# Performance work log

Hardware: AMD Instinct MI355X
Metric: run time of the kernel (lower is better)

The kernel has to match this reference:

```python
import jax, jax.numpy as jnp
import numpy as np

B, S, D, H, DK, DV = 2, 2048, 1024, 16, 64, 64
NEG_INF = -2.0**32 + 1.0  # matches torch module's self.inf


def setup_inputs() -> dict:
    key = jax.random.key(0)
    ks = jax.random.split(key, 9)
    sc = 0.02
    x = jax.random.normal(ks[0], (B, S, D), jnp.float32)
    Wq = jax.random.normal(ks[1], (D, H * DK), jnp.float32) * sc
    bq = jax.random.normal(ks[2], (H * DK,), jnp.float32) * sc
    Wk = jax.random.normal(ks[3], (D, H * DK), jnp.float32) * sc
    bk = jax.random.normal(ks[4], (H * DK,), jnp.float32) * sc
    Wv = jax.random.normal(ks[5], (D, H * DV), jnp.float32) * sc
    bv = jax.random.normal(ks[6], (H * DV,), jnp.float32) * sc
    Wo = jax.random.normal(ks[7], (H * DV, D), jnp.float32) * sc
    bo = jax.random.normal(ks[8], (D,), jnp.float32) * sc
    return {"x": x, "Wq": Wq, "bq": bq, "Wk": Wk, "bk": bk,
            "Wv": Wv, "bv": bv, "Wo": Wo, "bo": bo}


def reference(x, Wq, bq, Wk, bk, Wv, bv, Wo, bo):
    # stage == 'train' path: causal mask applied.
    b, s, _ = x.shape
    # chunk(heads, dim=-1) + cat(dim=0) in torch == per-head split; equivalent
    # math expressed as [B, S, H, d] with head-batched einsums.
    q = (x @ Wq + bq).reshape(b, s, H, DK)
    k = (x @ Wk + bk).reshape(b, s, H, DK)
    v = (x @ Wv + bv).reshape(b, s, H, DV)
    # NOTE: original module does NOT scale by 1/sqrt(dk) — stay faithful.
    score = jnp.einsum('bqhd,bkhd->bhqk', q, k)  # [B, H, S, S]
    causal = jnp.tril(jnp.ones((s, s), dtype=bool))
    score = jnp.where(causal, score, NEG_INF)
    attn = jax.nn.softmax(score, axis=-1)
    ctx = jnp.einsum('bhqk,bkhd->bqhd', attn, v).reshape(b, s, H * DV)
    return ctx @ Wo + bo
```

## Files before the change

### kernel.cpp

```cpp
#include <hip/hip_runtime.h>
#include <stdint.h>

typedef unsigned short u16;
typedef __bf16 bf16_t;
typedef bf16_t bf16x8 __attribute__((ext_vector_type(8)));
typedef float f32x4 __attribute__((ext_vector_type(4)));

#define SB 2048
#define DMODEL 1024
#define NH 16
#define HD 64

__device__ __forceinline__ u16 f2bf(float f) {
  union { float f; uint32_t u; } v; v.f = f;
  uint32_t u = v.u;
  return (u16)((u + 0x7FFFu + ((u >> 16) & 1u)) >> 16);
}

__device__ __forceinline__ void gload16(const void* g, void* l) {
  __builtin_amdgcn_global_load_lds((const __attribute__((address_space(1))) void*)g,
                                   (__attribute__((address_space(3))) void*)l, 16, 0, 0);
}


__global__ __launch_bounds__(256) void k_cvt_x(const float* __restrict__ x, u16* __restrict__ xb) {
  int i = blockIdx.x * 256 + threadIdx.x;
  float4 v = ((const float4*)x)[i];
  uint2 o;
  o.x = (unsigned)f2bf(v.x) | ((unsigned)f2bf(v.y) << 16);
  o.y = (unsigned)f2bf(v.z) | ((unsigned)f2bf(v.w) << 16);
  ((uint2*)xb)[i] = o;
}

__global__ __launch_bounds__(256) void k_transpose_w(
    const float* __restrict__ W0, const float* __restrict__ W1,
    const float* __restrict__ W2, const float* __restrict__ W3,
    u16* __restrict__ T0, u16* __restrict__ T1,
    u16* __restrict__ T2, u16* __restrict__ T3) {
  __shared__ float tile[32][33];
  int mat = blockIdx.z;
  const float* W = (mat == 0) ? W0 : (mat == 1) ? W1 : (mat == 2) ? W2 : W3;
  u16* T = (mat == 0) ? T0 : (mat == 1) ? T1 : (mat == 2) ? T2 : T3;
  int r0 = blockIdx.y * 32, c0 = blockIdx.x * 32;
  int tx = threadIdx.x & 31, ty = threadIdx.x >> 5;
#pragma unroll
  for (int j = 0; j < 4; ++j)
    tile[ty + j * 8][tx] = W[(size_t)(r0 + ty + j * 8) * DMODEL + c0 + tx];
  __syncthreads();
#pragma unroll
  for (int j = 0; j < 4; ++j)
    T[(size_t)(c0 + ty + j * 8) * DMODEL + r0 + tx] = f2bf(tile[tx][ty + j * 8]);
}


#define STG(MATBASE, LDS, SLOT, HALF, TK)                                          \
  do {                                                                             \
    _Pragma("unroll") for (int q_ = 0; q_ < 2; ++q_) {                             \
      int glin_ = tid + q_ * 512;                                                  \
      int row_ = glin_ >> 3;                                                       \
      int g_ = (glin_ & 7) ^ (row_ & 7);                                           \
      gload16(MATBASE + (size_t)((HALF) * 128 + row_) * DMODEL + (TK) * 64 + g_ * 8, \
              &LDS[SLOT][(HALF) * 8192 + glin_ * 8]);                              \
    }                                                                              \
  } while (0)

#define RDA(SLOT, MH)                                                     \
  do {                                                                    \
    _Pragma("unroll") for (int mm_ = 0; mm_ < 4; ++mm_) {                 \
      _Pragma("unroll") for (int kk_ = 0; kk_ < 2; ++kk_) {               \
        int row_ = wr * 128 + ((MH) * 4 + mm_) * 16 + l15;                \
        int g_ = (kk_ * 4 + grp) ^ (row_ & 7);                            \
        a[mm_][kk_] = *(const bf16x8*)&As[SLOT][row_ * 64 + g_ * 8];      \
      }                                                                   \
    }                                                                     \
  } while (0)

#define RDB(SLOT, NHF)                                                    \
  do {                                                                    \
    _Pragma("unroll") for (int nn_ = 0; nn_ < 2; ++nn_) {                 \
      _Pragma("unroll") for (int kk_ = 0; kk_ < 2; ++kk_) {               \
        int n_ = (NHF) * 2 + nn_;                                         \
        int row_ = wc * 64 + n_ * 16 + l15;                               \
        int g_ = (kk_ * 4 + grp) ^ (row_ & 7);                            \
        b[n_][kk_] = *(const bf16x8*)&Bs[SLOT][row_ * 64 + g_ * 8];       \
      }                                                                   \
    }                                                                     \
  } while (0)

#define MFM(MH, NHF)                                                                    \
  do {                                                                                  \
    _Pragma("unroll") for (int mm_ = 0; mm_ < 4; ++mm_) {                               \
      _Pragma("unroll") for (int nn_ = 0; nn_ < 2; ++nn_) {                             \
        _Pragma("unroll") for (int kk_ = 0; kk_ < 2; ++kk_) {                           \
          acc[(MH) * 4 + mm_][(NHF) * 2 + nn_] = __builtin_amdgcn_mfma_f32_16x16x32_bf16( \
              a[mm_][kk_], b[(NHF) * 2 + nn_][kk_], acc[(MH) * 4 + mm_][(NHF) * 2 + nn_], \
              0, 0, 0);                                                                 \
        }                                                                               \
      }                                                                                 \
    }                                                                                   \
  } while (0)

#define SBAR()                             \
  do {                                     \
    __builtin_amdgcn_sched_barrier(0);     \
    __builtin_amdgcn_s_barrier();          \
    __builtin_amdgcn_sched_barrier(0);     \
  } while (0)

#define LGKM0()                                           \
  do {                                                    \
    asm volatile("s_waitcnt lgkmcnt(0)" ::: "memory");    \
    __builtin_amdgcn_sched_barrier(0);                    \
  } while (0)

#define VMW(N)                                                \
  do {                                                        \
    asm volatile("s_waitcnt vmcnt(" #N ")" ::: "memory");     \
    __builtin_amdgcn_sched_barrier(0);                        \
  } while (0)

#define PHASE(RD0, RD1, ISS, MH, NHF, WAITC) \
  do {                                       \
    RD0;                                     \
    RD1;                                     \
    ISS;                                     \
    SBAR();                                  \
    LGKM0();                                 \
    __builtin_amdgcn_s_setprio(1);           \
    MFM(MH, NHF);                            \
    __builtin_amdgcn_s_setprio(0);           \
    WAITC;                                   \
    SBAR();                                  \
  } while (0)

__global__ __launch_bounds__(512, 2) void k_qkv8(
    const u16* __restrict__ xb, const u16* __restrict__ WqT, const u16* __restrict__ WkT,
    const u16* __restrict__ WvT, const float* __restrict__ bq, const float* __restrict__ bk,
    const float* __restrict__ bv, u16* __restrict__ Qg, u16* __restrict__ Kg,
    u16* __restrict__ VTg) {
  __shared__ u16 As[2][16384];
  __shared__ u16 Bs[2][16384];
  const int tid = threadIdx.x, w = tid >> 6, lane = tid & 63;
  const int l15 = lane & 15, grp = lane >> 4;
  const int wr = w >> 2, wc = w & 3;

  int id = blockIdx.x;
  id = (id & 7) * 24 + (id >> 3);
  const int role_v = (id >= 128);
  int mt, ntb;
  const u16 *Abase, *Bbase;
  if (!role_v) {
    mt = id >> 3;
    ntb = id & 7;
    Abase = xb + (size_t)mt * 256 * DMODEL;
    Bbase = (ntb < 4 ? WqT : WkT) + (size_t)(ntb & 3) * 256 * DMODEL;
  } else {
    int v = id - 128;
    mt = v >> 4;
    ntb = v & 15;
    Abase = WvT + (size_t)mt * 256 * DMODEL;
    Bbase = xb + (size_t)ntb * 256 * DMODEL;
  }

  f32x4 acc[8][4];
#pragma unroll
  for (int m = 0; m < 8; ++m)
#pragma unroll
    for (int n = 0; n < 4; ++n) acc[m][n] = (f32x4){0.f, 0.f, 0.f, 0.f};

  STG(Abase, As, 0, 0, 0);
  STG(Bbase, Bs, 0, 0, 0);
  STG(Abase, As, 0, 1, 0);
  STG(Bbase, Bs, 0, 1, 0);
  STG(Bbase, Bs, 1, 0, 1);
  STG(Abase, As, 1, 0, 1);
  VMW(4);
  SBAR();

  bf16x8 a[4][2], b[4][2];
#pragma unroll 1
  for (int it = 0; it < 8; ++it) {
    const int t0 = it * 2;
    const bool s2 = (t0 + 2) < 16, s3 = (t0 + 3) < 16;
    PHASE(RDA(0, 0), RDB(0, 0), STG(Bbase, Bs, 1, 1, t0 + 1), 0, 0, );
    PHASE(RDB(0, 1), , STG(Abase, As, 1, 1, t0 + 1), 0, 1, );
    PHASE(RDA(0, 1), , if (s2) STG(Bbase, Bs, 0, 0, t0 + 2), 1, 0, );
    PHASE(, , if (s2) STG(Abase, As, 0, 0, t0 + 2), 1, 1, if (s2) VMW(4); else VMW(0));
    PHASE(RDA(1, 0), RDB(1, 0), if (s2) STG(Bbase, Bs, 0, 1, t0 + 2), 0, 0, );
    PHASE(RDB(1, 1), , if (s2) STG(Abase, As, 0, 1, t0 + 2), 0, 1, );
    PHASE(RDA(1, 1), , if (s3) STG(Bbase, Bs, 1, 0, t0 + 3), 1, 0, );
    PHASE(, , if (s3) STG(Abase, As, 1, 0, t0 + 3), 1, 1, if (s3) VMW(4));
  }

#pragma unroll
  for (int m = 0; m < 8; ++m)
#pragma unroll
    for (int n = 0; n < 4; ++n)
#pragma unroll
      for (int r = 0; r < 4; ++r) {
        int mr = wr * 128 + m * 16 + 4 * grp + r;
        int nc = wc * 64 + n * 16 + l15;
        float v = acc[m][n][r];
        if (!role_v) {
          int Ng = ntb * 256 + nc;
          int col = Ng & 1023;
          float vb = v + (Ng < 1024 ? bq[col] : bk[col]);
          int mrow = mt * 256 + mr;
          int b_ = mrow >> 11, s_ = mrow & 2047, h_ = col >> 6, d_ = col & 63;
          u16* out = (Ng < 1024) ? Qg : Kg;
          out[((((size_t)b_ * NH + h_) * SB + s_) << 6) + d_] = f2bf(vb);
        } else {
          int vcf = mt * 256 + mr;
          int seq = ntb * 256 + nc;
          float vb = v + bv[vcf];
          int b2 = seq >> 11, key = seq & 2047, h2 = vcf >> 6, vc = vcf & 63;
          VTg[((((size_t)b2 * NH + h2) << 6) + vc) * SB + key] = f2bf(vb);
        }
      }
}


__device__ __forceinline__ void gemm_loop(const u16* __restrict__ A, const u16* __restrict__ Bt,
                                          u16* As, u16* Bs, f32x4 (&acc)[4][4], int m0) {
  const int t = threadIdx.x, w = t >> 6, lane = t & 63;
  const int l15 = lane & 15, grp = lane >> 4;
  const int wr = w >> 1, wc = w & 1;
#pragma unroll
  for (int i = 0; i < 4; ++i)
#pragma unroll
    for (int j = 0; j < 4; ++j) acc[i][j] = (f32x4){0.f, 0.f, 0.f, 0.f};

  for (int ks = 0; ks < 16; ++ks) {
    const int k0 = ks * 64;
#pragma unroll
    for (int j = 0; j < 4; ++j) {
      int glin = (w * 4 + j) * 64 + lane;
      int row = glin >> 3;
      int g = (glin & 7) ^ (row & 7);
      gload16(A + (size_t)(m0 + row) * DMODEL + k0 + g * 8, (char*)As + (size_t)(w * 4 + j) * 1024);
      gload16(Bt + (size_t)row * DMODEL + k0 + g * 8, (char*)Bs + (size_t)(w * 4 + j) * 1024);
    }
    __syncthreads();
#pragma unroll
    for (int kk = 0; kk < 2; ++kk) {
      bf16x8 af[4], bfr[4];
#pragma unroll
      for (int i = 0; i < 4; ++i) {
        int row = wr * 64 + i * 16 + l15;
        int g = (4 * kk + grp) ^ (row & 7);
        af[i] = *(const bf16x8*)((const char*)As + row * 128 + (g << 4));
      }
#pragma unroll
      for (int j = 0; j < 4; ++j) {
        int row = wc * 64 + j * 16 + l15;
        int g = (4 * kk + grp) ^ (row & 7);
        bfr[j] = *(const bf16x8*)((const char*)Bs + row * 128 + (g << 4));
      }
#pragma unroll
      for (int i = 0; i < 4; ++i)
#pragma unroll
        for (int j = 0; j < 4; ++j)
          acc[i][j] = __builtin_amdgcn_mfma_f32_16x16x32_bf16(af[i], bfr[j], acc[i][j], 0, 0, 0);
    }
    __syncthreads();
  }
}

__global__ __launch_bounds__(256) void k_gemm_o(
    const u16* __restrict__ ctx, const u16* __restrict__ WoT,
    const float* __restrict__ bo, float* __restrict__ out) {
  __shared__ u16 As[128 * 64];
  __shared__ u16 Bs[128 * 64];
  const int nt = blockIdx.x, mt = blockIdx.y;
  const int n0 = nt * 128;

  f32x4 acc[4][4];
  gemm_loop(ctx, WoT + (size_t)n0 * DMODEL, As, Bs, acc, mt * 128);

  const int t = threadIdx.x, w = t >> 6, lane = t & 63;
  const int l15 = lane & 15, grp = lane >> 4;
  const int wr = w >> 1, wc = w & 1;
#pragma unroll
  for (int i = 0; i < 4; ++i)
#pragma unroll
    for (int j = 0; j < 4; ++j)
#pragma unroll
      for (int r = 0; r < 4; ++r) {
        int mrow = mt * 128 + wr * 64 + i * 16 + 4 * grp + r;
        int ncol = n0 + wc * 64 + j * 16 + l15;
        out[(size_t)mrow * DMODEL + ncol] = acc[i][j][r] + bo[ncol];
      }
}


__global__ __launch_bounds__(256) void k_flash(const u16* __restrict__ Qg,
                                               const u16* __restrict__ Kg,
                                               const u16* __restrict__ VTg,
                                               u16* __restrict__ ctx) {
  __shared__ u16 Ks[2][64 * 64];
  __shared__ u16 VTs[2][64 * 64];
  __shared__ u16 Ps[4][16 * 64];
  const int linb = blockIdx.x;
  const int xcd = linb & 7, idx = linb >> 3;
  const int bh = xcd + ((idx & 3) << 3);
  const int pi = idx >> 2;
  const int t = threadIdx.x, w = t >> 6, lane = t & 63;
  const int l15 = lane & 15, grp = lane >> 4;
  const size_t bhS = (size_t)bh * SB;
  const u16* Kb = Kg + (bhS << 6);
  const u16* Vb = VTg + (bhS << 6);
  const int b = bh >> 4, h = bh & 15;

#pragma unroll 1
  for (int ph = 0; ph < 2; ++ph) {
    const int qt = ph ? 31 - pi : pi;
    const int qb = qt * 64;
    bf16x8 qf[2];
#pragma unroll
    for (int c = 0; c < 2; ++c)
      qf[c] = *(const bf16x8*)(Qg + ((bhS + qb + w * 16 + l15) << 6) + 32 * c + 8 * grp);
    f32x4 acc[4];
    float plsum[4];
#pragma unroll
    for (int ct = 0; ct < 4; ++ct) acc[ct] = (f32x4){0.f, 0.f, 0.f, 0.f};
#pragma unroll
    for (int j = 0; j < 4; ++j) plsum[j] = 0.f;

#pragma unroll
    for (int j = 0; j < 2; ++j) {
      int glin = w * 128 + j * 64 + lane;
      int row = glin >> 3;
      int g = (glin & 7) ^ (row & 7);
      gload16(Kb + ((size_t)row << 6) + g * 8, (char*)Ks[0] + w * 2048 + j * 1024);
      gload16(Vb + ((size_t)row << 11) + g * 8, (char*)VTs[0] + w * 2048 + j * 1024);
    }
    __syncthreads();
    int cur = 0;
    for (int kt = 0; kt <= qt; ++kt) {
      if (kt < qt) {
        const int kb2 = (kt + 1) * 64;
#pragma unroll
        for (int j = 0; j < 2; ++j) {
          int glin = w * 128 + j * 64 + lane;
          int row = glin >> 3;
          int g = (glin & 7) ^ (row & 7);
          gload16(Kb + ((size_t)(kb2 + row) << 6) + g * 8,
                  (char*)Ks[cur ^ 1] + w * 2048 + j * 1024);
          gload16(Vb + ((size_t)row << 11) + kb2 + g * 8,
                  (char*)VTs[cur ^ 1] + w * 2048 + j * 1024);
        }
      }
      f32x4 sc[4];
#pragma unroll
      for (int ct = 0; ct < 4; ++ct) {
        sc[ct] = (f32x4){0.f, 0.f, 0.f, 0.f};
#pragma unroll
        for (int c = 0; c < 2; ++c) {
          int row = ct * 16 + l15;
          int g = (4 * c + grp) ^ (row & 7);
          bf16x8 kf = *(const bf16x8*)((const char*)Ks[cur] + row * 128 + (g << 4));
          sc[ct] = __builtin_amdgcn_mfma_f32_16x16x32_bf16(qf[c], kf, sc[ct], 0, 0, 0);
        }
      }
      if (kt == qt) {
#pragma unroll
        for (int ct = 0; ct < 4; ++ct)
#pragma unroll
          for (int j = 0; j < 4; ++j) {
            int key = ct * 16 + l15, r = w * 16 + 4 * grp + j;
            if (key > r) sc[ct][j] = -1e30f;
          }
      }
#pragma unroll
      for (int ct = 0; ct < 4; ++ct)
#pragma unroll
        for (int j = 0; j < 4; ++j) {
          float p = __expf(sc[ct][j] - 32.0f);
          plsum[j] += p;
          int r = 4 * grp + j, cc = ct * 16 + l15;
          *(u16*)((char*)Ps[w] + r * 128 + (((cc >> 3) ^ (r & 7)) << 4) + (cc & 7) * 2) = f2bf(p);
        }
      asm volatile("s_waitcnt lgkmcnt(0)" ::: "memory");
      __builtin_amdgcn_sched_barrier(0);
#pragma unroll
      for (int ct = 0; ct < 4; ++ct) {
#pragma unroll
        for (int c2 = 0; c2 < 2; ++c2) {
          int pg = (4 * c2 + grp) ^ (l15 & 7);
          bf16x8 pf = *(const bf16x8*)((const char*)Ps[w] + l15 * 128 + (pg << 4));
          int vrow = ct * 16 + l15;
          int vg = (4 * c2 + grp) ^ (vrow & 7);
          bf16x8 vf = *(const bf16x8*)((const char*)VTs[cur] + vrow * 128 + (vg << 4));
          acc[ct] = __builtin_amdgcn_mfma_f32_16x16x32_bf16(pf, vf, acc[ct], 0, 0, 0);
        }
      }
      __syncthreads();
      cur ^= 1;
    }
#pragma unroll
    for (int j = 0; j < 4; ++j) {
#pragma unroll
      for (int d = 1; d < 16; d <<= 1) plsum[j] += __shfl_xor(plsum[j], d, 64);
      float inv = 1.f / plsum[j];
      int rg = qb + w * 16 + 4 * grp + j;
#pragma unroll
      for (int ct = 0; ct < 4; ++ct) {
        int col = h * 64 + ct * 16 + l15;
        ctx[((size_t)b * SB + rg) * DMODEL + col] = f2bf(acc[ct][j] * inv);
      }
    }
  }
}


extern "C" void kernel_launch(void* const* d_in, const int* in_sizes, int n_in,
                              void* d_out, int out_size, void* d_ws, size_t ws_size,
                              hipStream_t stream) {
  const float* x  = (const float*)d_in[0];
  const float* Wq = (const float*)d_in[1];
  const float* bq = (const float*)d_in[2];
  const float* Wk = (const float*)d_in[3];
  const float* bk = (const float*)d_in[4];
  const float* Wv = (const float*)d_in[5];
  const float* bv = (const float*)d_in[6];
  const float* Wo = (const float*)d_in[7];
  const float* bo = (const float*)d_in[8];
  float* out = (float*)d_out;

  char* ws = (char*)d_ws;
  u16* xb  = (u16*)(ws);
  u16* WqT = (u16*)(ws + (8ull  << 20));
  u16* WkT = (u16*)(ws + (10ull << 20));
  u16* WvT = (u16*)(ws + (12ull << 20));
  u16* WoT = (u16*)(ws + (14ull << 20));
  u16* Qg  = (u16*)(ws + (16ull << 20));
  u16* Kg  = (u16*)(ws + (24ull << 20));
  u16* VTg = (u16*)(ws + (32ull << 20));
  u16* ctx = (u16*)(ws + (40ull << 20));

  hipLaunchKernelGGL(k_cvt_x, dim3(4096), dim3(256), 0, stream, x, xb);
  hipLaunchKernelGGL(k_transpose_w, dim3(32, 32, 4), dim3(256), 0, stream,
                     Wq, Wk, Wv, Wo, WqT, WkT, WvT, WoT);
  hipLaunchKernelGGL(k_qkv8, dim3(192), dim3(512), 0, stream,
                     xb, WqT, WkT, WvT, bq, bk, bv, Qg, Kg, VTg);
  hipLaunchKernelGGL(k_flash, dim3(512), dim3(256), 0, stream, Qg, Kg, VTg, ctx);
  hipLaunchKernelGGL(k_gemm_o, dim3(8, 32), dim3(256), 0, stream, ctx, WoT, bo, out);
}
```

Measured before the change: 130.6 us.

## Use 128-row query tiles with 8 waves in flash attention kernel

The flash attention kernel now processes 128 query rows per block using 512 threads (8 waves), halving the grid to 256 blocks. Each K/V tile loaded into shared memory is therefore reused by twice as many query rows, and each thread issues one load per tile instead of two. The causal mask check becomes per-wave, since a 64-key tile may partly overlap a 128-row query block. Separately, sched_barrier fences around s_barrier and vmcnt waits in the QKV GEMM macros are dropped, and the output GEMM pointer arithmetic is simplified. The trade-offs are fewer resident blocks, and waves whose rows lie entirely below the last key tile doing wasted masked work on that tile.

After: 132.7 us. Within noise of the previous version (+1.6%).

```diff
diff --git a/kernel.cpp b/kernel.cpp
--- a/kernel.cpp
+++ b/kernel.cpp
@@ -100,12 +100,7 @@
     }                                                                                   \
   } while (0)
 
-#define SBAR()                             \
-  do {                                     \
-    __builtin_amdgcn_sched_barrier(0);     \
-    __builtin_amdgcn_s_barrier();          \
-    __builtin_amdgcn_sched_barrier(0);     \
-  } while (0)
+#define SBAR() __builtin_amdgcn_s_barrier()
 
 #define LGKM0()                                           \
   do {                                                    \
@@ -113,11 +108,7 @@
     __builtin_amdgcn_sched_barrier(0);                    \
   } while (0)
 
-#define VMW(N)                                                \
-  do {                                                        \
-    asm volatile("s_waitcnt vmcnt(" #N ")" ::: "memory");     \
-    __builtin_amdgcn_sched_barrier(0);                        \
-  } while (0)
+#define VMW(N) asm volatile("s_waitcnt vmcnt(" #N ")" ::: "memory")
 
 #define PHASE(RD0, RD1, ISS, MH, NHF, WAITC) \
   do {                                       \
@@ -221,7 +212,7 @@
 
 
 __device__ __forceinline__ void gemm_loop(const u16* __restrict__ A, const u16* __restrict__ Bt,
-                                          u16* As, u16* Bs, f32x4 (&acc)[4][4], int m0) {
+                                          u16* As, u16* Bs, f32x4 (&acc)[4][4]) {
   const int t = threadIdx.x, w = t >> 6, lane = t & 63;
   const int l15 = lane & 15, grp = lane >> 4;
   const int wr = w >> 1, wc = w & 1;
@@ -237,7 +228,7 @@
       int glin = (w * 4 + j) * 64 + lane;
       int row = glin >> 3;
       int g = (glin & 7) ^ (row & 7);
-      gload16(A + (size_t)(m0 + row) * DMODEL + k0 + g * 8, (char*)As + (size_t)(w * 4 + j) * 1024);
+      gload16(A + (size_t)row * DMODEL + k0 + g * 8, (char*)As + (size_t)(w * 4 + j) * 1024);
       gload16(Bt + (size_t)row * DMODEL + k0 + g * 8, (char*)Bs + (size_t)(w * 4 + j) * 1024);
     }
     __syncthreads();
@@ -272,10 +263,9 @@
   __shared__ u16 As[128 * 64];
   __shared__ u16 Bs[128 * 64];
   const int nt = blockIdx.x, mt = blockIdx.y;
-  const int n0 = nt * 128;
 
   f32x4 acc[4][4];
-  gemm_loop(ctx, WoT + (size_t)n0 * DMODEL, As, Bs, acc, mt * 128);
+  gemm_loop(ctx + (size_t)mt * 128 * DMODEL, WoT + (size_t)nt * 128 * DMODEL, As, Bs, acc);
 
   const int t = threadIdx.x, w = t >> 6, lane = t & 63;
   const int l15 = lane & 15, grp = lane >> 4;
@@ -287,19 +277,19 @@
 #pragma unroll
       for (int r = 0; r < 4; ++r) {
         int mrow = mt * 128 + wr * 64 + i * 16 + 4 * grp + r;
-        int ncol = n0 + wc * 64 + j * 16 + l15;
+        int ncol = nt * 128 + wc * 64 + j * 16 + l15;
         out[(size_t)mrow * DMODEL + ncol] = acc[i][j][r] + bo[ncol];
       }
 }
 
 
-__global__ __launch_bounds__(256) void k_flash(const u16* __restrict__ Qg,
+__global__ __launch_bounds__(512) void k_flash(const u16* __restrict__ Qg,
                                                const u16* __restrict__ Kg,
                                                const u16* __restrict__ VTg,
                                                u16* __restrict__ ctx) {
-  __shared__ u16 Ks[2][64 * 64];
-  __shared__ u16 VTs[2][64 * 64];
-  __shared__ u16 Ps[4][16 * 64];
+  __shared__ u16 Ks[2][4096];
+  __shared__ u16 VTs[2][4096];
+  __shared__ u16 Ps[8][1024];
   const int linb = blockIdx.x;
   const int xcd = linb & 7, idx = linb >> 3;
   const int bh = xcd + ((idx & 3) << 3);
@@ -313,8 +303,9 @@
 
 #pragma unroll 1
   for (int ph = 0; ph < 2; ++ph) {
-    const int qt = ph ? 31 - pi : pi;
-    const int qb = qt * 64;
+    const int qt = ph ? 15 - pi : pi;
+    const int qb = qt * 128;
+    const int nkt = 2 * qt + 2;
     bf16x8 qf[2];
 #pragma unroll
     for (int c = 0; c < 2; ++c)
@@ -326,29 +317,20 @@
 #pragma unroll
     for (int j = 0; j < 4; ++j) plsum[j] = 0.f;
 
-#pragma unroll
-    for (int j = 0; j < 2; ++j) {
-      int glin = w * 128 + j * 64 + lane;
-      int row = glin >> 3;
-      int g = (glin & 7) ^ (row & 7);
-      gload16(Kb + ((size_t)row << 6) + g * 8, (char*)Ks[0] + w * 2048 + j * 1024);
-      gload16(Vb + ((size_t)row << 11) + g * 8, (char*)VTs[0] + w * 2048 + j * 1024);
+    {
+      int row = t >> 3, g = (t & 7) ^ (row & 7);
+      gload16(Kb + ((size_t)row << 6) + g * 8, (char*)Ks[0] + t * 16);
+      gload16(Vb + ((size_t)row << 11) + g * 8, (char*)VTs[0] + t * 16);
     }
     __syncthreads();
     int cur = 0;
-    for (int kt = 0; kt <= qt; ++kt) {
-      if (kt < qt) {
-        const int kb2 = (kt + 1) * 64;
-#pragma unroll
-        for (int j = 0; j < 2; ++j) {
-          int glin = w * 128 + j * 64 + lane;
-          int row = glin >> 3;
-          int g = (glin & 7) ^ (row & 7);
-          gload16(Kb + ((size_t)(kb2 + row) << 6) + g * 8,
-                  (char*)Ks[cur ^ 1] + w * 2048 + j * 1024);
-          gload16(Vb + ((size_t)row << 11) + kb2 + g * 8,
-                  (char*)VTs[cur ^ 1] + w * 2048 + j * 1024);
-        }
+    for (int kt = 0; kt < nkt; ++kt) {
+      const int kb = kt * 64;
+      if (kt + 1 < nkt) {
+        int row = t >> 3, g = (t & 7) ^ (row & 7);
+        int kb2 = kb + 64;
+        gload16(Kb + ((size_t)(kb2 + row) << 6) + g * 8, (char*)Ks[cur ^ 1] + t * 16);
+        gload16(Vb + ((size_t)row << 11) + kb2 + g * 8, (char*)VTs[cur ^ 1] + t * 16);
       }
       f32x4 sc[4];
 #pragma unroll
@@ -362,12 +344,12 @@
           sc[ct] = __builtin_amdgcn_mfma_f32_16x16x32_bf16(qf[c], kf, sc[ct], 0, 0, 0);
         }
       }
-      if (kt == qt) {
+      if (kb + 63 >= qb + w * 16) {
 #pragma unroll
         for (int ct = 0; ct < 4; ++ct)
 #pragma unroll
           for (int j = 0; j < 4; ++j) {
-            int key = ct * 16 + l15, r = w * 16 + 4 * grp + j;
+            int key = kb + ct * 16 + l15, r = qb + w * 16 + 4 * grp + j;
             if (key > r) sc[ct][j] = -1e30f;
           }
       }
@@ -443,6 +425,6 @@
                      Wq, Wk, Wv, Wo, WqT, WkT, WvT, WoT);
   hipLaunchKernelGGL(k_qkv8, dim3(192), dim3(512), 0, stream,
                      xb, WqT, WkT, WvT, bq, bk, bv, Qg, Kg, VTg);
-  hipLaunchKernelGGL(k_flash, dim3(512), dim3(256), 0, stream, Qg, Kg, VTg, ctx);
+  hipLaunchKernelGGL(k_flash, dim3(256), dim3(512), 0, stream, Qg, Kg, VTg, ctx);
   hipLaunchKernelGGL(k_gemm_o, dim3(8, 32), dim3(256), 0, stream, ctx, WoT, bo, out);
 }
```
